# Kernel optimization log

Measured on AMD Instinct MI355X. Metric: run time of the kernel, lower is better.

The kernel has to match this reference:

```python
import jax, jax.numpy as jnp
import numpy as np

B, N, C, H = 2, 2048, 1024, 16
D = C // H  # head_dim = 64


def setup_inputs() -> dict:
    key = jax.random.key(0)
    k1, k2, k3, k4 = jax.random.split(key, 4)
    x = jax.random.normal(k1, (B, N, C), dtype=jnp.float32)
    # params (torch Linear: y = x @ W.T + b). Store as [in, out] for einsum.
    w_qkv = jax.random.normal(k2, (C, 3 * C), dtype=jnp.float32) * (1.0 / np.sqrt(C))
    w_out = jax.random.normal(k3, (C, C), dtype=jnp.float32) * (1.0 / np.sqrt(C))
    b_out = jax.random.normal(k4, (C,), dtype=jnp.float32) * 0.01
    # causal mask: 1 above the diagonal -> masked_fill(-inf)
    attn_mask = jnp.triu(jnp.ones((N, N), dtype=jnp.int32), k=1)
    return {"x": x, "w_qkv": w_qkv, "w_out": w_out, "b_out": b_out, "attn_mask": attn_mask}


def reference(x, w_qkv, w_out, b_out, attn_mask):
    b, n, c = x.shape
    scale = 1.0 / jnp.sqrt(jnp.asarray(D, dtype=x.dtype))
    qkv = jnp.einsum('bnc,cd->bnd', x, w_qkv)                # [B, N, 3C]
    qkv = qkv.reshape(b, n, 3, H, D)
    q = qkv[:, :, 0].transpose(0, 2, 1, 3)                   # [B, H, N, D]
    k = qkv[:, :, 1].transpose(0, 2, 1, 3)
    v = qkv[:, :, 2].transpose(0, 2, 1, 3)
    scores = jnp.einsum('bhqd,bhkd->bhqk', q, k) * scale     # [B, H, N, N]
    scores = jnp.where(attn_mask == 1, jnp.asarray(-jnp.inf, dtype=scores.dtype), scores)
    attn = jax.nn.softmax(scores, axis=-1)
    # dropout is identity in eval mode (deterministic reference)
    out = jnp.einsum('bhqk,bhkd->bhqd', attn, v)             # [B, H, N, D]
    out = out.transpose(0, 2, 1, 3).reshape(b, n, c)         # [B, N, C]
    return jnp.einsum('bnc,cd->bnd', out, w_out) + b_out
```

## Files before the change

kernel.cpp:

```cpp
#include <hip/hip_runtime.h>

typedef _Float16 f16;
typedef _Float16 f16x8 __attribute__((ext_vector_type(8)));
typedef _Float16 f16x4 __attribute__((ext_vector_type(4)));
typedef float    f32x4 __attribute__((ext_vector_type(4)));

#define MFMA16(a, b, c) __builtin_amdgcn_mfma_f32_16x16x32_f16((a), (b), (c), 0, 0, 0)

__device__ __forceinline__ void gload16(const void* g, void* l) {
  __builtin_amdgcn_global_load_lds(
      (const __attribute__((address_space(1))) unsigned int*)g,
      (__attribute__((address_space(3))) unsigned int*)l, 16, 0, 0);
}

__device__ __forceinline__ float ex2(float x) {
  float r;
  asm("v_exp_f32 %0, %1" : "=v"(r) : "v"(x));
  return r;
}

#define WAITV(N) asm volatile("s_waitcnt vmcnt(" #N ")" ::: "memory")
#define BARRIER() __builtin_amdgcn_s_barrier()
#define CFENCE() asm volatile("" ::: "memory")


__global__ void cast_f32_f16(const float* __restrict__ in, f16* __restrict__ out, int n4) {
  int i = blockIdx.x * blockDim.x + threadIdx.x;
  if (i < n4) {
    float4 v = ((const float4*)in)[i];
    f16x4 o;
    o.x = (f16)v.x; o.y = (f16)v.y; o.z = (f16)v.z; o.w = (f16)v.w;
    ((f16x4*)out)[i] = o;
  }
}

__global__ void transpose_cast2(const float* __restrict__ wqkv, f16* __restrict__ oqkv,
                                const float* __restrict__ wout, f16* __restrict__ oout) {
  __shared__ float tile[32][33];
  int bx = blockIdx.x;
  const float* in;
  f16* out;
  int Cc, c0;
  if (bx < 96) { in = wqkv; out = oqkv; Cc = 3072; c0 = bx * 32; }
  else         { in = wout; out = oout; Cc = 1024; c0 = (bx - 96) * 32; }
  int r0 = blockIdx.y * 32;
  int tx = threadIdx.x, ty = threadIdx.y;
#pragma unroll
  for (int i = ty; i < 32; i += 8)
    tile[i][tx] = in[(size_t)(r0 + i) * Cc + c0 + tx];
  __syncthreads();
#pragma unroll
  for (int i = ty; i < 32; i += 8)
    out[(size_t)(c0 + i) * 1024 + r0 + tx] = (f16)tile[tx][i];
}

template <int KDIM>
__device__ __forceinline__ void gemm_core(const f16* __restrict__ A, const f16* __restrict__ Bt,
                                          int bm, int bn, f16* lA, f16* lB, f32x4 acc[4][4]) {
  const int t = threadIdx.x, lane = t & 63, wave = t >> 6;
  const int wm = wave >> 1, wn = wave & 1;
  const int srow = lane >> 3;
  const int skb = (lane & 7) * 16;
  const int nkt = KDIM / 64;
  for (int kt = 0; kt < nkt; ++kt) {
    __syncthreads();
#pragma unroll
    for (int c = 0; c < 4; ++c) {
      int cc = c * 4 + wave;
      int row = cc * 8 + srow;
      int kbs = skb ^ ((row & 7) << 4);
      gload16((const char*)A + (size_t)(bm * 128 + row) * (KDIM * 2) + kt * 128 + kbs,
              lA + cc * 512);
      gload16((const char*)Bt + (size_t)(bn * 128 + row) * (KDIM * 2) + kt * 128 + kbs,
              lB + cc * 512);
    }
    __syncthreads();
#pragma unroll
    for (int ks = 0; ks < 2; ++ks) {
      f16x8 af[4], bf[4];
#pragma unroll
      for (int mi = 0; mi < 4; ++mi) {
        int r = wm * 64 + mi * 16 + (lane & 15);
        int ke = (ks * 32 + ((lane >> 4) << 3)) ^ ((r & 7) << 3);
        af[mi] = *(const f16x8*)&lA[r * 64 + ke];
      }
#pragma unroll
      for (int ni = 0; ni < 4; ++ni) {
        int r = wn * 64 + ni * 16 + (lane & 15);
        int ke = (ks * 32 + ((lane >> 4) << 3)) ^ ((r & 7) << 3);
        bf[ni] = *(const f16x8*)&lB[r * 64 + ke];
      }
#pragma unroll
      for (int mi = 0; mi < 4; ++mi)
#pragma unroll
        for (int ni = 0; ni < 4; ++ni)
          acc[mi][ni] = MFMA16(af[mi], bf[ni], acc[mi][ni]);
    }
  }
}

__global__ __launch_bounds__(256, 2) void gemm_qkv(const f16* __restrict__ A,
                                                   const f16* __restrict__ Bt,
                                                   f16* __restrict__ Qo, f16* __restrict__ Ko,
                                                   f16* __restrict__ Vt) {
  __shared__ __align__(16) f16 smem[128 * 136];
  f16* lA = smem;
  f16* lB = smem + 8192;
  f32x4 acc[4][4] = {};
  int w = blockIdx.x;
  int xcd = w & 7, i = w >> 3;
  int xr = xcd >> 1, xc = xcd & 1;
  int bm = xr * 8 + (i & 7);
  int bn = xc * 12 + (i >> 3);
  gemm_core<1024>(A, Bt, bm, bn, lA, lB, acc);
  int lane = threadIdx.x & 63, wave = threadIdx.x >> 6;
  int wm = wave >> 1, wn = wave & 1;
  int g = lane >> 4, q15 = lane & 15;
  int sec = (bn * 128) >> 10;
  if (sec < 2) {
    float scl = (sec == 0) ? 0.18033688f : 1.0f;
#pragma unroll
    for (int mi = 0; mi < 4; ++mi)
#pragma unroll
      for (int ni = 0; ni < 4; ++ni)
#pragma unroll
        for (int reg = 0; reg < 4; ++reg) {
          int gr = bm * 128 + wm * 64 + mi * 16 + (g << 2) + reg;
          int gc = bn * 128 + wn * 64 + ni * 16 + q15;
          int b = gr >> 11, n = gr & 2047;
          int jj = gc & 1023;
          int h = jj >> 6, d = jj & 63;
          f16 v = (f16)(acc[mi][ni][reg] * scl);
          size_t bh = (size_t)(b * 16 + h);
          if (sec == 0) Qo[(bh * 2048 + n) * 64 + d] = v;
          else          Ko[(bh * 2048 + n) * 64 + d] = v;
        }
  } else {
    __syncthreads();
#pragma unroll
    for (int mi = 0; mi < 4; ++mi)
#pragma unroll
      for (int ni = 0; ni < 4; ++ni)
#pragma unroll
        for (int reg = 0; reg < 4; ++reg) {
          int rl = wm * 64 + mi * 16 + (g << 2) + reg;
          int cl = wn * 64 + ni * 16 + q15;
          int r5 = rl & 31;
          int rlp = (rl & ~31) | (((r5 >> 2) & 3) << 3) | (((r5 >> 4) & 1) << 2) | (r5 & 3);
          smem[cl * 136 + rlp] = (f16)acc[mi][ni][reg];
        }
    __syncthreads();
    int tid = threadIdx.x;
    int cl = tid >> 1, half = tid & 1;
    int jj = (bn * 128 + cl) & 1023;
    int h = jj >> 6, d = jj & 63;
    int b = (bm * 128) >> 11;
    size_t bh = (size_t)(b * 16 + h);
    f16* dst = Vt + (bh * 64 + d) * 2048 + (bm * 128 & 2047) + half * 64;
    const f16* src = smem + cl * 136 + half * 64;
#pragma unroll
    for (int j8 = 0; j8 < 8; ++j8)
      *(f16x8*)&dst[j8 * 8] = *(const f16x8*)&src[j8 * 8];
  }
}

__device__ __forceinline__ void attn_one(const f16* __restrict__ Qb, const f16* __restrict__ Kb,
                                         const f16* __restrict__ Vb, f16* __restrict__ Ob,
                                         int qt, int lane, int wave, f16* lK, f16* lV) {
  const int N = 2048;
  const int wq0 = qt * 64 + wave * 16;
  const int g = lane >> 4, q15 = lane & 15;
  f16x8 qf[2];
#pragma unroll
  for (int ks = 0; ks < 2; ++ks)
    qf[ks] = *(const f16x8*)&Qb[(size_t)(wq0 + q15) * 64 + ks * 32 + (g << 3)];
  f32x4 oacc[4] = {};
  float mrun = -1e30f, lrun = 0.f;
  const int srow = lane >> 3, skb = (lane & 7) * 16;
  const int ntiles = qt + 1;

  auto STAGE = [&](int buf, int kv) {
    int kv0 = kv << 6;
#pragma unroll
    for (int c = 0; c < 2; ++c) {
      int cc = c * 4 + wave;
      int row = cc * 8 + srow;
      int kbs = skb ^ ((row & 7) << 4);
      gload16((const char*)Kb + (size_t)(kv0 + row) * 128 + kbs, lK + buf * 4096 + cc * 512);
      gload16((const char*)Vb + (size_t)row * (N * 2) + (size_t)kv0 * 2 + kbs,
              lV + buf * 4096 + cc * 512);
    }
  };

  STAGE(0, 0);
  if (ntiles > 1) STAGE(1, 1);
  for (int kv = 0; kv < ntiles; ++kv) {
    int cur = kv & 1;
    if (kv + 1 < ntiles) WAITV(4); else WAITV(0);
    BARRIER();
    const f16* K0 = lK + cur * 4096;
    const f16* V0 = lV + cur * 4096;
    int kv0 = kv << 6;
    f32x4 s[4] = {};
    __builtin_amdgcn_s_setprio(1);
#pragma unroll
    for (int ks = 0; ks < 2; ++ks) {
      f16x8 kf[4];
#pragma unroll
      for (int ni = 0; ni < 4; ++ni) {
        int r = ni * 16 + q15;
        int ke = (ks * 32 + (g << 3)) ^ ((r & 7) << 3);
        kf[ni] = *(const f16x8*)&K0[r * 64 + ke];
      }
#pragma unroll
      for (int ni = 0; ni < 4; ++ni) s[ni] = MFMA16(kf[ni], qf[ks], s[ni]);
    }
    __builtin_amdgcn_s_setprio(0);
    if (kv == qt) {
      int gq = wq0 + q15;
#pragma unroll
      for (int ni = 0; ni < 4; ++ni)
#pragma unroll
        for (int reg = 0; reg < 4; ++reg) {
          int gk = kv0 + ni * 16 + g * 4 + reg;
          if (gk > gq) s[ni][reg] = -1e30f;
        }
    }
    f32x4 m4 = s[0];
#pragma unroll
    for (int ni = 1; ni < 4; ++ni)
#pragma unroll
      for (int reg = 0; reg < 4; ++reg) m4[reg] = fmaxf(m4[reg], s[ni][reg]);
    float mx = fmaxf(fmaxf(m4[0], m4[1]), fmaxf(m4[2], m4[3]));
    mx = fmaxf(mx, __shfl_xor(mx, 16));
    mx = fmaxf(mx, __shfl_xor(mx, 32));
    if (__any(mx > mrun)) {
      float mnew = fmaxf(mrun, mx);
      float corr = ex2(mrun - mnew);
      mrun = mnew;
      lrun *= corr;
#pragma unroll
      for (int ni = 0; ni < 4; ++ni)
#pragma unroll
        for (int reg = 0; reg < 4; ++reg) oacc[ni][reg] *= corr;
    }
#pragma unroll
    for (int ni = 0; ni < 4; ++ni)
#pragma unroll
      for (int reg = 0; reg < 4; ++reg) s[ni][reg] = ex2(s[ni][reg] - mrun);
    f32x4 racc = (s[0] + s[1]) + (s[2] + s[3]);
    float rsum = (racc[0] + racc[1]) + (racc[2] + racc[3]);
    rsum += __shfl_xor(rsum, 16);
    rsum += __shfl_xor(rsum, 32);
    lrun += rsum;
    f16x8 pf[2];
#pragma unroll
    for (int ks = 0; ks < 2; ++ks)
#pragma unroll
      for (int e = 0; e < 8; ++e) pf[ks][e] = (f16)s[2 * ks + (e >> 2)][e & 3];
    __builtin_amdgcn_s_setprio(1);
#pragma unroll
    for (int ks = 0; ks < 2; ++ks) {
      f16x8 vf[4];
#pragma unroll
      for (int mi = 0; mi < 4; ++mi) {
        int r = mi * 16 + q15;
        int ke = (ks * 32 + (g << 3)) ^ ((r & 7) << 3);
        vf[mi] = *(const f16x8*)&V0[r * 64 + ke];
      }
#pragma unroll
      for (int mi = 0; mi < 4; ++mi) oacc[mi] = MFMA16(vf[mi], pf[ks], oacc[mi]);
    }
    __builtin_amdgcn_s_setprio(0);
    BARRIER();
    CFENCE();
    if (kv + 2 < ntiles) STAGE(cur, kv + 2);
  }
  float inv = 1.0f / lrun;
  int gq = wq0 + q15;
#pragma unroll
  for (int mi = 0; mi < 4; ++mi) {
    f16x4 o4;
#pragma unroll
    for (int reg = 0; reg < 4; ++reg) o4[reg] = (f16)(oacc[mi][reg] * inv);
    *(f16x4*)&Ob[(size_t)gq * 1024 + mi * 16 + g * 4] = o4;
  }
}

__global__ __launch_bounds__(256, 4) void attn(const f16* __restrict__ Q,
                                               const f16* __restrict__ K,
                                               const f16* __restrict__ Vt,
                                               f16* __restrict__ O) {
  __shared__ __align__(16) f16 lK[2 * 4096];
  __shared__ __align__(16) f16 lV[2 * 4096];
  int w = blockIdx.x;
  int c = w & 7, j = w >> 3;
  int a = j >> 5, k = j & 31;
  int bh = c * 4 + a;
  int kk = (a >= 2) ? ((k + 8) & 31) : k;
  int qt = (a & 1) ? (31 - kk) : kk;
  int b = bh >> 4, h = bh & 15;
  int lane = threadIdx.x & 63, wave = threadIdx.x >> 6;
  const f16* Qb = Q + (size_t)bh * 2048 * 64;
  const f16* Kb = K + (size_t)bh * 2048 * 64;
  const f16* Vb = Vt + (size_t)bh * 2048 * 64;
  f16* Ob = O + (size_t)b * 2048 * 1024 + h * 64;
  attn_one(Qb, Kb, Vb, Ob, qt, lane, wave, lK, lV);
}

__global__ __launch_bounds__(256, 2) void gemm_out(const f16* __restrict__ A,
                                                   const f16* __restrict__ Bt,
                                                   const float* __restrict__ bias,
                                                   float* __restrict__ out) {
  __shared__ __align__(16) f16 lA[128 * 64];
  __shared__ __align__(16) f16 lB[128 * 64];
  f32x4 acc[4][4] = {};
  int w = blockIdx.x;
  int xcd = w & 7, i = w >> 3;
  int bm = xcd * 4 + (i & 3);
  int bn = i >> 2;
  gemm_core<1024>(A, Bt, bm, bn, lA, lB, acc);
  int lane = threadIdx.x & 63, wave = threadIdx.x >> 6;
  int wm = wave >> 1, wn = wave & 1;
#pragma unroll
  for (int mi = 0; mi < 4; ++mi)
#pragma unroll
    for (int ni = 0; ni < 4; ++ni)
#pragma unroll
      for (int reg = 0; reg < 4; ++reg) {
        int gr = bm * 128 + wm * 64 + mi * 16 + ((lane >> 4) << 2) + reg;
        int gc = bn * 128 + wn * 64 + ni * 16 + (lane & 15);
        out[(size_t)gr * 1024 + gc] = acc[mi][ni][reg] + bias[gc];
      }
}

extern "C" void kernel_launch(void* const* d_in, const int* in_sizes, int n_in,
                              void* d_out, int out_size, void* d_ws, size_t ws_size,
                              hipStream_t stream) {
  const float* x     = (const float*)d_in[0];
  const float* w_qkv = (const float*)d_in[1];
  const float* w_out = (const float*)d_in[2];
  const float* b_out = (const float*)d_in[3];
  float* out = (float*)d_out;
  char* ws = (char*)d_ws;

  f16* xh    = (f16*)(ws);
  f16* wqkvT = (f16*)(ws + (8u << 20));
  f16* woutT = (f16*)(ws + (14u << 20));
  f16* Qs    = (f16*)(ws + (16u << 20));
  f16* Ks    = (f16*)(ws + (24u << 20));
  f16* Vts   = (f16*)(ws + (32u << 20));
  f16* Oa    = (f16*)(ws + (40u << 20));

  cast_f32_f16<<<4096, 256, 0, stream>>>(x, xh, 1048576);
  transpose_cast2<<<dim3(128, 32), dim3(32, 8), 0, stream>>>(w_qkv, wqkvT, w_out, woutT);
  gemm_qkv<<<768, 256, 0, stream>>>(xh, wqkvT, Qs, Ks, Vts);
  attn<<<1024, 256, 0, stream>>>(Qs, Ks, Vts, Oa);
  gemm_out<<<256, 256, 0, stream>>>(Oa, woutT, b_out, out);
}
```

Baseline: 106.8 us.

## Double-buffer GEMM K-loop with async LDS loads and merge prep kernels

The shared GEMM core now uses 32-wide K tiles with two LDS buffers. Global-to-LDS loads for tile kt+2 are issued while tile kt is being computed, with vmcnt waits replacing the full syncthreads pairs, and the MFMA block is raised in wave priority. The cast and transpose-cast kernels are merged into one prep launch to save launch overhead. In exchange, the smaller K tile means more barriers per GEMM, and the swizzle changes to match the 64-byte rows.

```diff
diff --git a/kernel.cpp b/kernel.cpp
--- a/kernel.cpp
+++ b/kernel.cpp
@@ -23,28 +23,28 @@
 #define BARRIER() __builtin_amdgcn_s_barrier()
 #define CFENCE() asm volatile("" ::: "memory")
 
-
-__global__ void cast_f32_f16(const float* __restrict__ in, f16* __restrict__ out, int n4) {
-  int i = blockIdx.x * blockDim.x + threadIdx.x;
-  if (i < n4) {
-    float4 v = ((const float4*)in)[i];
+__global__ void prep(const float* __restrict__ x, f16* __restrict__ xh,
+                     const float* __restrict__ wqkv, f16* __restrict__ oqkv,
+                     const float* __restrict__ wout, f16* __restrict__ oout) {
+  __shared__ float tile[32][33];
+  int bx = blockIdx.x, t = threadIdx.x;
+  if (bx < 4096) {
+    int i = bx * 256 + t;
+    float4 v = ((const float4*)x)[i];
     f16x4 o;
     o.x = (f16)v.x; o.y = (f16)v.y; o.z = (f16)v.z; o.w = (f16)v.w;
-    ((f16x4*)out)[i] = o;
-  }
-}
-
-__global__ void transpose_cast2(const float* __restrict__ wqkv, f16* __restrict__ oqkv,
-                                const float* __restrict__ wout, f16* __restrict__ oout) {
-  __shared__ float tile[32][33];
-  int bx = blockIdx.x;
+    ((f16x4*)xh)[i] = o;
+    return;
+  }
+  int tb = bx - 4096;
+  int bx2 = tb & 127, by = tb >> 7;
   const float* in;
   f16* out;
   int Cc, c0;
-  if (bx < 96) { in = wqkv; out = oqkv; Cc = 3072; c0 = bx * 32; }
-  else         { in = wout; out = oout; Cc = 1024; c0 = (bx - 96) * 32; }
-  int r0 = blockIdx.y * 32;
-  int tx = threadIdx.x, ty = threadIdx.y;
+  if (bx2 < 96) { in = wqkv; out = oqkv; Cc = 3072; c0 = bx2 * 32; }
+  else          { in = wout; out = oout; Cc = 1024; c0 = (bx2 - 96) * 32; }
+  int r0 = by * 32;
+  int tx = t & 31, ty = t >> 5;
 #pragma unroll
   for (int i = ty; i < 32; i += 8)
     tile[i][tx] = in[(size_t)(r0 + i) * Cc + c0 + tx];
@@ -59,43 +59,55 @@
                                           int bm, int bn, f16* lA, f16* lB, f32x4 acc[4][4]) {
   const int t = threadIdx.x, lane = t & 63, wave = t >> 6;
   const int wm = wave >> 1, wn = wave & 1;
-  const int srow = lane >> 3;
-  const int skb = (lane & 7) * 16;
-  const int nkt = KDIM / 64;
+  const int q15 = lane & 15, g = lane >> 4;
+  const int srow = lane >> 2;
+  const int sgr = lane & 3;
+  const int nkt = KDIM / 32;
+
+  auto STAGE = [&](int buf, int kt) {
+#pragma unroll
+    for (int c = 0; c < 2; ++c) {
+      int cc = c * 4 + wave;
+      int row = cc * 16 + srow;
+      int kbs = (sgr ^ ((row >> 1) & 3)) * 16;
+      gload16((const char*)A + (size_t)(bm * 128 + row) * (KDIM * 2) + kt * 64 + kbs,
+              lA + buf * 4096 + cc * 512);
+      gload16((const char*)Bt + (size_t)(bn * 128 + row) * (KDIM * 2) + kt * 64 + kbs,
+              lB + buf * 4096 + cc * 512);
+    }
+  };
+
+  STAGE(0, 0);
+  STAGE(1, 1);
   for (int kt = 0; kt < nkt; ++kt) {
-    __syncthreads();
-#pragma unroll
-    for (int c = 0; c < 4; ++c) {
-      int cc = c * 4 + wave;
-      int row = cc * 8 + srow;
-      int kbs = skb ^ ((row & 7) << 4);
-      gload16((const char*)A + (size_t)(bm * 128 + row) * (KDIM * 2) + kt * 128 + kbs,
-              lA + cc * 512);
-      gload16((const char*)Bt + (size_t)(bn * 128 + row) * (KDIM * 2) + kt * 128 + kbs,
-              lB + cc * 512);
-    }
-    __syncthreads();
-#pragma unroll
-    for (int ks = 0; ks < 2; ++ks) {
-      f16x8 af[4], bf[4];
-#pragma unroll
-      for (int mi = 0; mi < 4; ++mi) {
-        int r = wm * 64 + mi * 16 + (lane & 15);
-        int ke = (ks * 32 + ((lane >> 4) << 3)) ^ ((r & 7) << 3);
-        af[mi] = *(const f16x8*)&lA[r * 64 + ke];
-      }
-#pragma unroll
-      for (int ni = 0; ni < 4; ++ni) {
-        int r = wn * 64 + ni * 16 + (lane & 15);
-        int ke = (ks * 32 + ((lane >> 4) << 3)) ^ ((r & 7) << 3);
-        bf[ni] = *(const f16x8*)&lB[r * 64 + ke];
-      }
-#pragma unroll
-      for (int mi = 0; mi < 4; ++mi)
-#pragma unroll
-        for (int ni = 0; ni < 4; ++ni)
-          acc[mi][ni] = MFMA16(af[mi], bf[ni], acc[mi][ni]);
-    }
+    int cur = kt & 1;
+    if (kt + 1 < nkt) WAITV(4); else WAITV(0);
+    BARRIER();
+    const f16* A0 = lA + cur * 4096;
+    const f16* B0 = lB + cur * 4096;
+    f16x8 af[4], bf[4];
+#pragma unroll
+    for (int mi = 0; mi < 4; ++mi) {
+      int r = wm * 64 + mi * 16 + q15;
+      int ke = (g << 3) ^ (((r >> 1) & 3) << 3);
+      af[mi] = *(const f16x8*)&A0[r * 32 + ke];
+    }
+#pragma unroll
+    for (int ni = 0; ni < 4; ++ni) {
+      int r = wn * 64 + ni * 16 + q15;
+      int ke = (g << 3) ^ (((r >> 1) & 3) << 3);
+      bf[ni] = *(const f16x8*)&B0[r * 32 + ke];
+    }
+    __builtin_amdgcn_s_setprio(1);
+#pragma unroll
+    for (int mi = 0; mi < 4; ++mi)
+#pragma unroll
+      for (int ni = 0; ni < 4; ++ni)
+        acc[mi][ni] = MFMA16(af[mi], bf[ni], acc[mi][ni]);
+    __builtin_amdgcn_s_setprio(0);
+    BARRIER();
+    CFENCE();
+    if (kt + 2 < nkt) STAGE(cur, kt + 2);
   }
 }
 
@@ -312,8 +324,8 @@
                                                    const f16* __restrict__ Bt,
                                                    const float* __restrict__ bias,
                                                    float* __restrict__ out) {
-  __shared__ __align__(16) f16 lA[128 * 64];
-  __shared__ __align__(16) f16 lB[128 * 64];
+  __shared__ __align__(16) f16 lA[2 * 4096];
+  __shared__ __align__(16) f16 lB[2 * 4096];
   f32x4 acc[4][4] = {};
   int w = blockIdx.x;
   int xcd = w & 7, i = w >> 3;
@@ -352,8 +364,7 @@
   f16* Vts   = (f16*)(ws + (32u << 20));
   f16* Oa    = (f16*)(ws + (40u << 20));
 
-  cast_f32_f16<<<4096, 256, 0, stream>>>(x, xh, 1048576);
-  transpose_cast2<<<dim3(128, 32), dim3(32, 8), 0, stream>>>(w_qkv, wqkvT, w_out, woutT);
+  prep<<<4096 + 128 * 32, 256, 0, stream>>>(x, xh, w_qkv, wqkvT, w_out, woutT);
   gemm_qkv<<<768, 256, 0, stream>>>(xh, wqkvT, Qs, Ks, Vts);
   attn<<<1024, 256, 0, stream>>>(Qs, Ks, Vts, Oa);
   gemm_out<<<256, 256, 0, stream>>>(Oa, woutT, b_out, out);
```

After: 109.2 us. 1.02x slower.

## Merge prep kernels into one launch and halve out-GEMM M tile

Applied to the files above, without the earlier changes.

The separate x-cast and weight transpose-cast kernels are merged into a single prep launch, with block index ranges choosing the role. This removes one kernel launch and the gap between the two. The output projection GEMM now uses 64x128 tiles instead of 128x128, so the grid grows from 256 to 512 blocks and fills the GPU's CUs better. In exchange each block reuses its B tile less and issues more global loads per MFMA.

```diff
diff --git a/kernel.cpp b/kernel.cpp
--- a/kernel.cpp
+++ b/kernel.cpp
@@ -23,28 +23,28 @@
 #define BARRIER() __builtin_amdgcn_s_barrier()
 #define CFENCE() asm volatile("" ::: "memory")
 
-
-__global__ void cast_f32_f16(const float* __restrict__ in, f16* __restrict__ out, int n4) {
-  int i = blockIdx.x * blockDim.x + threadIdx.x;
-  if (i < n4) {
-    float4 v = ((const float4*)in)[i];
+__global__ void prep(const float* __restrict__ x, f16* __restrict__ xh,
+                     const float* __restrict__ wqkv, f16* __restrict__ oqkv,
+                     const float* __restrict__ wout, f16* __restrict__ oout) {
+  __shared__ float tile[32][33];
+  int bx = blockIdx.x, t = threadIdx.x;
+  if (bx < 4096) {
+    int i = bx * 256 + t;
+    float4 v = ((const float4*)x)[i];
     f16x4 o;
     o.x = (f16)v.x; o.y = (f16)v.y; o.z = (f16)v.z; o.w = (f16)v.w;
-    ((f16x4*)out)[i] = o;
-  }
-}
-
-__global__ void transpose_cast2(const float* __restrict__ wqkv, f16* __restrict__ oqkv,
-                                const float* __restrict__ wout, f16* __restrict__ oout) {
-  __shared__ float tile[32][33];
-  int bx = blockIdx.x;
+    ((f16x4*)xh)[i] = o;
+    return;
+  }
+  int tb = bx - 4096;
+  int bx2 = tb & 127, by = tb >> 7;
   const float* in;
   f16* out;
   int Cc, c0;
-  if (bx < 96) { in = wqkv; out = oqkv; Cc = 3072; c0 = bx * 32; }
-  else         { in = wout; out = oout; Cc = 1024; c0 = (bx - 96) * 32; }
-  int r0 = blockIdx.y * 32;
-  int tx = threadIdx.x, ty = threadIdx.y;
+  if (bx2 < 96) { in = wqkv; out = oqkv; Cc = 3072; c0 = bx2 * 32; }
+  else          { in = wout; out = oout; Cc = 1024; c0 = (bx2 - 96) * 32; }
+  int r0 = by * 32;
+  int tx = t & 31, ty = t >> 5;
 #pragma unroll
   for (int i = ty; i < 32; i += 8)
     tile[i][tx] = in[(size_t)(r0 + i) * Cc + c0 + tx];
@@ -92,6 +92,57 @@
       }
 #pragma unroll
       for (int mi = 0; mi < 4; ++mi)
+#pragma unroll
+        for (int ni = 0; ni < 4; ++ni)
+          acc[mi][ni] = MFMA16(af[mi], bf[ni], acc[mi][ni]);
+    }
+  }
+}
+
+template <int KDIM>
+__device__ __forceinline__ void gemm_core64(const f16* __restrict__ A, const f16* __restrict__ Bt,
+                                            int bm, int bn, f16* lA, f16* lB, f32x4 acc[2][4]) {
+  const int t = threadIdx.x, lane = t & 63, wave = t >> 6;
+  const int wm = wave >> 1, wn = wave & 1;
+  const int srow = lane >> 3;
+  const int skb = (lane & 7) * 16;
+  const int nkt = KDIM / 64;
+  for (int kt = 0; kt < nkt; ++kt) {
+    __syncthreads();
+#pragma unroll
+    for (int c = 0; c < 2; ++c) {
+      int cc = c * 4 + wave;
+      int row = cc * 8 + srow;
+      int kbs = skb ^ ((row & 7) << 4);
+      gload16((const char*)A + (size_t)(bm * 64 + row) * (KDIM * 2) + kt * 128 + kbs,
+              lA + cc * 512);
+    }
+#pragma unroll
+    for (int c = 0; c < 4; ++c) {
+      int cc = c * 4 + wave;
+      int row = cc * 8 + srow;
+      int kbs = skb ^ ((row & 7) << 4);
+      gload16((const char*)Bt + (size_t)(bn * 128 + row) * (KDIM * 2) + kt * 128 + kbs,
+              lB + cc * 512);
+    }
+    __syncthreads();
+#pragma unroll
+    for (int ks = 0; ks < 2; ++ks) {
+      f16x8 af[2], bf[4];
+#pragma unroll
+      for (int mi = 0; mi < 2; ++mi) {
+        int r = wm * 32 + mi * 16 + (lane & 15);
+        int ke = (ks * 32 + ((lane >> 4) << 3)) ^ ((r & 7) << 3);
+        af[mi] = *(const f16x8*)&lA[r * 64 + ke];
+      }
+#pragma unroll
+      for (int ni = 0; ni < 4; ++ni) {
+        int r = wn * 64 + ni * 16 + (lane & 15);
+        int ke = (ks * 32 + ((lane >> 4) << 3)) ^ ((r & 7) << 3);
+        bf[ni] = *(const f16x8*)&lB[r * 64 + ke];
+      }
+#pragma unroll
+      for (int mi = 0; mi < 2; ++mi)
 #pragma unroll
         for (int ni = 0; ni < 4; ++ni)
           acc[mi][ni] = MFMA16(af[mi], bf[ni], acc[mi][ni]);
@@ -312,23 +363,24 @@
                                                    const f16* __restrict__ Bt,
                                                    const float* __restrict__ bias,
                                                    float* __restrict__ out) {
-  __shared__ __align__(16) f16 lA[128 * 64];
-  __shared__ __align__(16) f16 lB[128 * 64];
-  f32x4 acc[4][4] = {};
+  __shared__ __align__(16) f16 smem[12288];
+  f16* lA = smem;
+  f16* lB = smem + 4096;
+  f32x4 acc[2][4] = {};
   int w = blockIdx.x;
   int xcd = w & 7, i = w >> 3;
-  int bm = xcd * 4 + (i & 3);
-  int bn = i >> 2;
-  gemm_core<1024>(A, Bt, bm, bn, lA, lB, acc);
+  int bm = xcd * 8 + (i & 7);
+  int bn = i >> 3;
+  gemm_core64<1024>(A, Bt, bm, bn, lA, lB, acc);
   int lane = threadIdx.x & 63, wave = threadIdx.x >> 6;
   int wm = wave >> 1, wn = wave & 1;
 #pragma unroll
-  for (int mi = 0; mi < 4; ++mi)
+  for (int mi = 0; mi < 2; ++mi)
 #pragma unroll
     for (int ni = 0; ni < 4; ++ni)
 #pragma unroll
       for (int reg = 0; reg < 4; ++reg) {
-        int gr = bm * 128 + wm * 64 + mi * 16 + ((lane >> 4) << 2) + reg;
+        int gr = bm * 64 + wm * 32 + mi * 16 + ((lane >> 4) << 2) + reg;
         int gc = bn * 128 + wn * 64 + ni * 16 + (lane & 15);
         out[(size_t)gr * 1024 + gc] = acc[mi][ni][reg] + bias[gc];
       }
@@ -352,9 +404,8 @@
   f16* Vts   = (f16*)(ws + (32u << 20));
   f16* Oa    = (f16*)(ws + (40u << 20));
 
-  cast_f32_f16<<<4096, 256, 0, stream>>>(x, xh, 1048576);
-  transpose_cast2<<<dim3(128, 32), dim3(32, 8), 0, stream>>>(w_qkv, wqkvT, w_out, woutT);
+  prep<<<4096 + 128 * 32, 256, 0, stream>>>(x, xh, w_qkv, wqkvT, w_out, woutT);
   gemm_qkv<<<768, 256, 0, stream>>>(xh, wqkvT, Qs, Ks, Vts);
   attn<<<1024, 256, 0, stream>>>(Qs, Ks, Vts, Oa);
-  gemm_out<<<256, 256, 0, stream>>>(Oa, woutT, b_out, out);
-}
+  gemm_out<<<512, 256, 0, stream>>>(Oa, woutT, b_out, out);
+}
```

Result: faster. 100.8 us, median of 4 (-5.6%).
